# Optimization experiments

Hardware: AMD Instinct MI355X
Metric: run time of the kernel (lower is better)

## Reference

```python
import jax, jax.numpy as jnp
import numpy as np

B, T, C, H = 4, 2048, 768, 12
D = C // H  # head dim = 64
EPS = 1e-5


def setup_inputs() -> dict:
    key = jax.random.key(0)
    ks = jax.random.split(key, 12)
    s = lambda fan_in: 1.0 / np.sqrt(fan_in)
    return {
        "x": jax.random.normal(ks[0], (B, T, C), dtype=jnp.float32),
        "ln1_g": jnp.ones((C,), jnp.float32),
        "ln1_b": jnp.zeros((C,), jnp.float32),
        "w_attn": jax.random.normal(ks[1], (C, 3 * C), jnp.float32) * s(C),
        "b_attn": jnp.zeros((3 * C,), jnp.float32),
        "w_aproj": jax.random.normal(ks[2], (C, C), jnp.float32) * s(C),
        "b_aproj": jnp.zeros((C,), jnp.float32),
        "ln2_g": jnp.ones((C,), jnp.float32),
        "ln2_b": jnp.zeros((C,), jnp.float32),
        "w_fc": jax.random.normal(ks[3], (C, 4 * C), jnp.float32) * s(C),
        "b_fc": jnp.zeros((4 * C,), jnp.float32),
        "w_mproj": jax.random.normal(ks[4], (4 * C, C), jnp.float32) * s(4 * C),
        "b_mproj": jnp.zeros((C,), jnp.float32),
    }


def _layernorm(x, g, b):
    mu = jnp.mean(x, axis=-1, keepdims=True)
    var = jnp.mean(jnp.square(x - mu), axis=-1, keepdims=True)
    return (x - mu) * jax.lax.rsqrt(var + EPS) * g + b


def _attention(h, w_attn, b_attn, w_aproj, b_aproj):
    qkv = h @ w_attn + b_attn                          # [B,T,3C]
    q, k, v = jnp.split(qkv, 3, axis=-1)
    q = q.reshape(B, T, H, D)
    k = k.reshape(B, T, H, D)
    v = v.reshape(B, T, H, D)
    att = jnp.einsum("bqhd,bkhd->bhqk", q, k) * (1.0 / np.sqrt(D))
    causal = jnp.tril(jnp.ones((T, T), bool))
    att = jnp.where(causal, att, -jnp.inf)
    att = jax.nn.softmax(att, axis=-1)
    y = jnp.einsum("bhqk,bkhd->bqhd", att, v).reshape(B, T, C)
    return y @ w_aproj + b_aproj


def reference(x, ln1_g, ln1_b, w_attn, b_attn, w_aproj, b_aproj,
              ln2_g, ln2_b, w_fc, b_fc, w_mproj, b_mproj):
    x = x + _attention(_layernorm(x, ln1_g, ln1_b), w_attn, b_attn, w_aproj, b_aproj)
    h = _layernorm(x, ln2_g, ln2_b)
    h = jax.nn.gelu(h @ w_fc + b_fc, approximate=True)  # tanh approximation, matches F.gelu(approximate='tanh')
    x = x + (h @ w_mproj + b_mproj)
    return x
```

## Files before the change

kernel.cpp:

```cpp
#include <hip/hip_runtime.h>


typedef unsigned short ushortT;
typedef unsigned int uintT;
typedef __attribute__((ext_vector_type(8))) __bf16 bf16x8;
typedef __attribute__((ext_vector_type(4))) float f32x4;

#define MFMA16(a, b, c) __builtin_amdgcn_mfma_f32_16x16x32_bf16(a, b, c, 0, 0, 0)

__device__ inline float b2f(ushortT u) {
  return __uint_as_float(((uintT)u) << 16);
}
__device__ inline ushortT f2b(float f) {
  uintT x = __float_as_uint(f);
  uintT r = x + 0x7fffu + ((x >> 16) & 1u);
  return (ushortT)(r >> 16);
}
__device__ inline uintT pack_bf2(float a, float b) {
  return __builtin_amdgcn_perm(__float_as_uint(b), __float_as_uint(a),
                               0x07060302u);
}

__device__ inline float fast_exp2(float x) {
#if __has_builtin(__builtin_amdgcn_exp2f)
  return __builtin_amdgcn_exp2f(x);
#else
  return exp2f(x);
#endif
}

__device__ inline float gelu_tanh(float v) {
  float t = 0.7978845608028654f * (v + 0.044715f * v * v * v);
  return v / (1.0f + __expf(-2.0f * t));
}

__device__ __forceinline__ void glds16(const ushortT* g, ushortT* l) {
  __builtin_amdgcn_global_load_lds(
      (const __attribute__((address_space(1))) unsigned int*)(const void*)g,
      (__attribute__((address_space(3))) unsigned int*)(void*)l, 16, 0, 0);
}

__global__ __launch_bounds__(256) void detect_dtype(
    const ushortT* __restrict__ w, int* __restrict__ flag) {
  __shared__ int red;
  if (threadIdx.x == 0) red = 0;
  __syncthreads();
  int crazy = 0;
  for (int i = threadIdx.x; i < 4096; i += 256) {
    uintT e = (w[2 * i] >> 7) & 0xFF;
    if (e >= 150) crazy = 1;
  }
  if (crazy) atomicOr(&red, 1);
  __syncthreads();
  if (threadIdx.x == 0) *flag = red;
}

struct VecArgs {
  const void* src[8];
  int n[8];
  int dstoff[8];
};
__global__ __launch_bounds__(256) void convert_vecs(
    VecArgs a, ushortT* __restrict__ pv, const int* __restrict__ flag) {
  int fl = *flag;
  int t = blockIdx.y;
  int i = blockIdx.x * 256 + threadIdx.x;
  if (i >= a.n[t]) return;
  float v = fl ? ((const float*)a.src[t])[i] : b2f(((const ushortT*)a.src[t])[i]);
  pv[a.dstoff[t] + i] = f2b(v);
}

__global__ __launch_bounds__(256) void transpose_any(
    const void* __restrict__ in, ushortT* __restrict__ out, int K, int N,
    const int* __restrict__ flag) {
  __shared__ ushortT t[32][33];
  int fl = *flag;
  int n0 = blockIdx.x * 32, k0 = blockIdx.y * 32;
  int x = threadIdx.x, y0 = threadIdx.y;
#pragma unroll
  for (int i = y0; i < 32; i += 8) {
    size_t idx = (size_t)(k0 + i) * N + n0 + x;
    t[i][x] = fl ? f2b(((const float*)in)[idx]) : ((const ushortT*)in)[idx];
  }
  __syncthreads();
#pragma unroll
  for (int i = y0; i < 32; i += 8)
    out[(size_t)(n0 + i) * K + k0 + x] = t[x][i];
}

__global__ __launch_bounds__(256) void vtrans_kernel(
    const ushortT* __restrict__ qkv, ushortT* __restrict__ vt) {
  const int T = 2048, C3 = 2304;
  __shared__ ushortT tile[64][65];
  int bh = blockIdx.y;
  int b = bh / 12, h = bh % 12;
  int t0 = blockIdx.x * 64;
  int col = threadIdx.x & 63, rowi = threadIdx.x >> 6;
#pragma unroll
  for (int rr = rowi; rr < 64; rr += 4)
    tile[rr][col] =
        qkv[((size_t)(b * T + t0 + rr)) * C3 + 1536 + h * 64 + col];
  __syncthreads();
#pragma unroll
  for (int dd = rowi; dd < 64; dd += 4)
    vt[((size_t)bh * 64 + dd) * T + t0 + col] = tile[col][dd];
}

template <int MODE>
__global__ __launch_bounds__(256) void ln_kernel(
    const void* __restrict__ xin, const ushortT* __restrict__ g,
    const ushortT* __restrict__ bb, ushortT* __restrict__ out,
    const int* __restrict__ flag) {
  const int C = 768;
  bool f32;
  if constexpr (MODE == 1) f32 = true; else f32 = (*flag != 0);
  size_t base = (size_t)blockIdx.x * C;
  int tid = threadIdx.x;
  const float* xf = (const float*)xin;
  const ushortT* xb = (const ushortT*)xin;
  float v0 = f32 ? xf[base + tid]       : b2f(xb[base + tid]);
  float v1 = f32 ? xf[base + tid + 256] : b2f(xb[base + tid + 256]);
  float v2 = f32 ? xf[base + tid + 512] : b2f(xb[base + tid + 512]);
  float s = v0 + v1 + v2;
  float q = v0 * v0 + v1 * v1 + v2 * v2;
#pragma unroll
  for (int off = 32; off; off >>= 1) {
    s += __shfl_xor(s, off);
    q += __shfl_xor(q, off);
  }
  __shared__ float as_[4], aq_[4];
  if ((tid & 63) == 0) { as_[tid >> 6] = s; aq_[tid >> 6] = q; }
  __syncthreads();
  s = as_[0] + as_[1] + as_[2] + as_[3];
  q = aq_[0] + aq_[1] + aq_[2] + aq_[3];
  float mu = s * (1.0f / 768.0f);
  float var = q * (1.0f / 768.0f) - mu * mu;
  float rs = rsqrtf(var + 1e-5f);
  ushortT* orow = out + base;
  orow[tid]       = f2b((v0 - mu) * rs * b2f(g[tid])       + b2f(bb[tid]));
  orow[tid + 256] = f2b((v1 - mu) * rs * b2f(g[tid + 256]) + b2f(bb[tid + 256]));
  orow[tid + 512] = f2b((v2 - mu) * rs * b2f(g[tid + 512]) + b2f(bb[tid + 512]));
}

template <int EPI>
__global__ __launch_bounds__(256) void gemm_sb(
    const ushortT* __restrict__ A, const ushortT* __restrict__ Bt,
    const ushortT* __restrict__ bias, const void* __restrict__ res,
    void* __restrict__ out, int N, int K, int nbm, int nbn,
    const int* __restrict__ flag) {
  __shared__ ushortT As[128 * 64];
  __shared__ ushortT Bs[128 * 64];
  int fl = (EPI >= 2) ? *flag : 0;
  int tid = threadIdx.x;
  int lane = tid & 63, wave = tid >> 6;
  int quad = lane >> 4, n = lane & 15, n7 = n & 7;
  int wm = (wave >> 1) * 64, wn = (wave & 1) * 64;
  int l = blockIdx.x;
  int xcd = l & 7, j = l >> 3;
  int m0 = (xcd * (nbm >> 3) + j / nbn) * 128;
  int n0 = (j % nbn) * 128;

  int trow = tid >> 3;
  int tc = ((tid & 7) ^ (trow & 7)) << 3;
  const ushortT* ga = A + (size_t)(m0 + trow) * K + tc;
  const ushortT* gb = Bt + (size_t)(n0 + trow) * K + tc;
  const int ldst = wave * 512;

  const int c0 = (quad ^ n7) << 3;
  const int c1 = ((4 + quad) ^ n7) << 3;
  const int arow = (wm + n) * 64;
  const int brow = (wn + n) * 64;

  f32x4 acc[4][4] = {};

  for (int k0 = 0; k0 < K; k0 += 64) {
    __syncthreads();
#pragma unroll
    for (int i = 0; i < 4; ++i)
      glds16(ga + (size_t)(i * 32) * K + k0, As + ldst + i * 2048);
#pragma unroll
    for (int i = 0; i < 4; ++i)
      glds16(gb + (size_t)(i * 32) * K + k0, Bs + ldst + i * 2048);
    __syncthreads();

    bf16x8 af[4][2], bfr[4][2];
#pragma unroll
    for (int mi = 0; mi < 4; ++mi) {
      af[mi][0] = *(const bf16x8*)(As + arow + mi * 1024 + c0);
      af[mi][1] = *(const bf16x8*)(As + arow + mi * 1024 + c1);
    }
#pragma unroll
    for (int ni = 0; ni < 4; ++ni) {
      bfr[ni][0] = *(const bf16x8*)(Bs + brow + ni * 1024 + c0);
      bfr[ni][1] = *(const bf16x8*)(Bs + brow + ni * 1024 + c1);
    }
#pragma unroll
    for (int mi = 0; mi < 4; ++mi)
#pragma unroll
      for (int ni = 0; ni < 4; ++ni) {
        acc[mi][ni] = MFMA16(af[mi][0], bfr[ni][0], acc[mi][ni]);
        acc[mi][ni] = MFMA16(af[mi][1], bfr[ni][1], acc[mi][ni]);
      }
  }

#pragma unroll
  for (int mi = 0; mi < 4; ++mi) {
#pragma unroll
    for (int ni = 0; ni < 4; ++ni) {
      int gc = n0 + wn + ni * 16 + n;
      float bv = b2f(bias[gc]);
      int gr0 = m0 + wm + mi * 16 + quad * 4;
#pragma unroll
      for (int r = 0; r < 4; ++r) {
        size_t idx = (size_t)(gr0 + r) * N + gc;
        float v = acc[mi][ni][r] + bv;
        if constexpr (EPI == 1) v = gelu_tanh(v);
        if constexpr (EPI == 2) {
          v += fl ? ((const float*)res)[idx] : b2f(((const ushortT*)res)[idx]);
          ((float*)out)[idx] = v;
        } else if constexpr (EPI == 3) {
          v += ((const float*)res)[idx];
          if (fl) ((float*)out)[idx] = v;
          else    ((ushortT*)out)[idx] = f2b(v);
        } else {
          ((ushortT*)out)[idx] = f2b(v);
        }
      }
    }
  }
}

__global__ __launch_bounds__(256) void attn_kernel(
    const ushortT* __restrict__ qkv, const ushortT* __restrict__ vt,
    ushortT* __restrict__ y) {
  const int T = 2048, C3 = 2304;
  constexpr int LDP = 72;
  __shared__ ushortT Ks[2][64 * 64];
  __shared__ ushortT Vs[2][64 * 64];
  __shared__ ushortT Ps[4 * 16 * LDP];
  int bh = blockIdx.y;
  int b = bh / 12, h = bh % 12;
  int pj = blockIdx.x;
  int tid = threadIdx.x;
  int lane = tid & 63, wave = tid >> 6;
  int quad = lane >> 4, n = lane & 15, n7 = n & 7;

  const ushortT* base = qkv + (size_t)b * T * C3;
  const ushortT* kbase = base + 768 + h * 64;
  const ushortT* vbase = vt + (size_t)bh * 64 * T;
  ushortT* myP = Ps + wave * 16 * LDP;

  const float QS = 0.18033688011112042f;
  const float MB = 20.0f;

  int qtA = pj, qtB = 31 - pj;
  int nA = qtA + 1, ntot = 33;

  int srow = lane >> 3, scol = lane & 7;
  const ushortT* kg =
      kbase + (size_t)(wave * 16 + srow) * C3 + ((scol ^ srow) << 3);
  const ushortT* vg =
      vbase + (size_t)(wave * 16 + srow) * T + ((scol ^ srow) << 3);

  const int c0 = (quad ^ n7) << 3;
  const int c1 = ((4 + quad) ^ n7) << 3;

  int qt = qtA;
  int qw = qt * 64 + wave * 16;
  bf16x8 aq[2];
  {
    const ushortT* qrow = base + (size_t)(qw + n) * C3 + h * 64 + quad * 8;
#pragma unroll
    for (int dh = 0; dh < 2; ++dh) {
      union { ushortT u[8]; bf16x8 v; } tmp;
#pragma unroll
      for (int j = 0; j < 8; ++j) tmp.u[j] = f2b(b2f(qrow[dh * 32 + j]) * QS);
      aq[dh] = tmp.v;
    }
  }
  f32x4 Ot[4] = {};
  float l_ = 0.f;

  auto stage = [&](int kt_, int buf) {
    int kof = kt_ << 6;
    ushortT* lk = &Ks[buf][0] + wave * 1024;
    ushortT* lv = &Vs[buf][0] + wave * 1024;
    glds16(kg + (size_t)kof * C3, lk);
    glds16(kg + (size_t)(kof + 8) * C3, lk + 512);
    glds16(vg + kof, lv);
    glds16(vg + (size_t)8 * T + kof, lv + 512);
  };

  stage(0, 0);
  __syncthreads();

  int cur = 0;
  for (int t = 0; t < ntot; ++t) {
    int kt = (t < nA) ? t : t - nA;
    if (t + 1 < ntot) {
      int ktn = (t + 1 < nA) ? t + 1 : t + 1 - nA;
      stage(ktn, cur ^ 1);
    }
    const ushortT* ks = &Ks[cur][0];
    const ushortT* vs = &Vs[cur][0];

    f32x4 St[4];
#pragma unroll
    for (int g = 0; g < 4; ++g) {
      bf16x8 ka0 = *(const bf16x8*)(ks + (g * 16 + n) * 64 + c0);
      bf16x8 ka1 = *(const bf16x8*)(ks + (g * 16 + n) * 64 + c1);
      f32x4 z = {};
      z = MFMA16(ka0, aq[0], z);
      St[g] = MFMA16(ka1, aq[1], z);
    }
    if (kt == qt) {
      int lim = wave * 16 + n;
#pragma unroll
      for (int g = 0; g < 4; ++g)
#pragma unroll
        for (int r = 0; r < 4; ++r)
          if (g * 16 + quad * 4 + r > lim) St[g][r] = -1e30f;
    }
    float ls = 0.f;
#pragma unroll
    for (int g = 0; g < 4; ++g) {
      float p0 = fast_exp2(St[g][0] - MB);
      float p1 = fast_exp2(St[g][1] - MB);
      float p2 = fast_exp2(St[g][2] - MB);
      float p3 = fast_exp2(St[g][3] - MB);
      ls += (p0 + p1) + (p2 + p3);
      uint2 pk;
      pk.x = pack_bf2(p0, p1);
      pk.y = pack_bf2(p2, p3);
      *(uint2*)(myP + n * LDP + g * 16 + quad * 4) = pk;
    }
    ls += __shfl_xor(ls, 16);
    ls += __shfl_xor(ls, 32);
    l_ += ls;

    bf16x8 pb0 = *(const bf16x8*)(myP + n * LDP + quad * 8);
    bf16x8 pb1 = *(const bf16x8*)(myP + n * LDP + 32 + quad * 8);
#pragma unroll
    for (int dt = 0; dt < 4; ++dt) {
      bf16x8 va0 = *(const bf16x8*)(vs + (dt * 16 + n) * 64 + c0);
      bf16x8 va1 = *(const bf16x8*)(vs + (dt * 16 + n) * 64 + c1);
      Ot[dt] = MFMA16(va0, pb0, Ot[dt]);
      Ot[dt] = MFMA16(va1, pb1, Ot[dt]);
    }

    if (kt == qt) {
      float inv = 1.0f / l_;
      int qg = qw + n;
#pragma unroll
      for (int dt = 0; dt < 4; ++dt) {
        uint2 o;
        o.x = pack_bf2(Ot[dt][0] * inv, Ot[dt][1] * inv);
        o.y = pack_bf2(Ot[dt][2] * inv, Ot[dt][3] * inv);
        *(uint2*)(y + (size_t)(b * T + qg) * 768 + h * 64 + dt * 16 +
                  quad * 4) = o;
      }
      if (t + 1 < ntot) {
        qt = qtB;
        qw = qt * 64 + wave * 16;
        const ushortT* qrow =
            base + (size_t)(qw + n) * C3 + h * 64 + quad * 8;
#pragma unroll
        for (int dh = 0; dh < 2; ++dh) {
          union { ushortT u[8]; bf16x8 v; } tmp;
#pragma unroll
          for (int j = 0; j < 8; ++j)
            tmp.u[j] = f2b(b2f(qrow[dh * 32 + j]) * QS);
          aq[dh] = tmp.v;
        }
#pragma unroll
        for (int dt = 0; dt < 4; ++dt)
#pragma unroll
          for (int r = 0; r < 4; ++r) Ot[dt][r] = 0.f;
        l_ = 0.f;
      }
    }
    __syncthreads();
    cur ^= 1;
  }
}

extern "C" void kernel_launch(void* const* d_in, const int* in_sizes, int n_in,
                              void* d_out, int out_size, void* d_ws,
                              size_t ws_size, hipStream_t stream) {
  (void)in_sizes; (void)n_in; (void)out_size; (void)ws_size;
  const void* x       = d_in[0];
  const void* w_attn  = d_in[3];
  const void* w_aproj = d_in[5];
  const void* w_fc    = d_in[9];
  const void* w_mproj = d_in[11];

  char* ws = (char*)d_ws;
  ushortT* h1  = (ushortT*)(ws);
  ushortT* qkv = (ushortT*)(ws + 12582912);
  ushortT* yb  = (ushortT*)(ws + 50331648);
  float*   x1  = (float*)(ws + 62914560);
  ushortT* fcg = (ushortT*)(ws + 88080384);
  ushortT* wT0 = (ushortT*)(ws + 138412032);
  ushortT* wT1 = (ushortT*)(ws + 141950976);
  ushortT* wT2 = (ushortT*)(ws + 143130624);
  ushortT* wT3 = (ushortT*)(ws + 147849216);
  ushortT* pv  = (ushortT*)(ws + 152567808);
  int*     flag = (int*)(ws + 152600576);
  ushortT* vt  = h1;
  ushortT* h2  = yb;

  const int O_LN1G = 0, O_LN1B = 768, O_BATT = 1536, O_BAPR = 3840,
            O_LN2G = 4608, O_LN2B = 5376, O_BFC = 6144, O_BMPR = 9216;

  detect_dtype<<<1, 256, 0, stream>>>((const ushortT*)w_fc, flag);

  VecArgs va;
  va.src[0] = d_in[1];  va.n[0] = 768;  va.dstoff[0] = O_LN1G;
  va.src[1] = d_in[2];  va.n[1] = 768;  va.dstoff[1] = O_LN1B;
  va.src[2] = d_in[4];  va.n[2] = 2304; va.dstoff[2] = O_BATT;
  va.src[3] = d_in[6];  va.n[3] = 768;  va.dstoff[3] = O_BAPR;
  va.src[4] = d_in[7];  va.n[4] = 768;  va.dstoff[4] = O_LN2G;
  va.src[5] = d_in[8];  va.n[5] = 768;  va.dstoff[5] = O_LN2B;
  va.src[6] = d_in[10]; va.n[6] = 3072; va.dstoff[6] = O_BFC;
  va.src[7] = d_in[12]; va.n[7] = 768;  va.dstoff[7] = O_BMPR;
  convert_vecs<<<dim3(12, 8), 256, 0, stream>>>(va, pv, flag);

  dim3 tb(32, 8);
  transpose_any<<<dim3(72, 24), tb, 0, stream>>>(w_attn, wT0, 768, 2304, flag);
  transpose_any<<<dim3(24, 24), tb, 0, stream>>>(w_aproj, wT1, 768, 768, flag);
  transpose_any<<<dim3(96, 24), tb, 0, stream>>>(w_fc, wT2, 768, 3072, flag);
  transpose_any<<<dim3(24, 96), tb, 0, stream>>>(w_mproj, wT3, 3072, 768, flag);

  ln_kernel<0><<<8192, 256, 0, stream>>>(x, pv + O_LN1G, pv + O_LN1B, h1, flag);
  gemm_sb<0><<<1152, 256, 0, stream>>>(
      h1, wT0, pv + O_BATT, nullptr, qkv, 2304, 768, 64, 18, flag);
  vtrans_kernel<<<dim3(32, 48), 256, 0, stream>>>(qkv, vt);
  attn_kernel<<<dim3(16, 48), 256, 0, stream>>>(qkv, vt, yb);
  gemm_sb<2><<<384, 256, 0, stream>>>(
      yb, wT1, pv + O_BAPR, x, x1, 768, 768, 64, 6, flag);
  ln_kernel<1><<<8192, 256, 0, stream>>>(x1, pv + O_LN2G, pv + O_LN2B, h2, flag);
  gemm_sb<1><<<1536, 256, 0, stream>>>(
      h2, wT2, pv + O_BFC, nullptr, fcg, 3072, 768, 64, 24, flag);
  gemm_sb<3><<<384, 256, 0, stream>>>(
      fcg, wT3, pv + O_BMPR, x1, d_out, 768, 3072, 64, 6, flag);
}
```

Baseline: 438.0 us.

## Replace GEMM with triple-buffered pipelined kernel and wider 128x256 tiles

Replaces the single-buffered GEMM with one that cycles three LDS buffers over 32-wide K tiles. The next-but-one tile's global-to-LDS loads are issued while MFMAs run on the current tile, with explicit vmcnt waits and raised wave priority around the MFMAs. The QKV and FC GEMMs move to 128x256 block tiles with occupancy hinted at two blocks per CU. This aims to hide global load latency and improve operand reuse, at the cost of more LDS, more registers and more complex barrier and waitcnt logic.

```diff
diff --git a/kernel.cpp b/kernel.cpp
--- a/kernel.cpp
+++ b/kernel.cpp
@@ -142,71 +142,128 @@
   orow[tid + 512] = f2b((v2 - mu) * rs * b2f(g[tid + 512]) + b2f(bb[tid + 512]));
 }
 
-template <int EPI>
-__global__ __launch_bounds__(256) void gemm_sb(
+template <int EPI, int BN>
+__global__ __launch_bounds__(256, 2) void gemm_8p(
     const ushortT* __restrict__ A, const ushortT* __restrict__ Bt,
     const ushortT* __restrict__ bias, const void* __restrict__ res,
     void* __restrict__ out, int N, int K, int nbm, int nbn,
     const int* __restrict__ flag) {
-  __shared__ ushortT As[128 * 64];
-  __shared__ ushortT Bs[128 * 64];
+  constexpr int MI = (BN == 256) ? 8 : 4;
+  constexpr int NI = 4;
+  constexpr int LOADS = 2 + BN / 64;
+  __shared__ ushortT As3[3][128 * 32];
+  __shared__ ushortT Bs3[3][BN * 32];
   int fl = (EPI >= 2) ? *flag : 0;
   int tid = threadIdx.x;
   int lane = tid & 63, wave = tid >> 6;
-  int quad = lane >> 4, n = lane & 15, n7 = n & 7;
-  int wm = (wave >> 1) * 64, wn = (wave & 1) * 64;
+  int quad = lane >> 4, n = lane & 15;
+  int wm, wn;
+  if constexpr (BN == 256) { wm = 0; wn = wave * 64; }
+  else { wm = (wave >> 1) * 64; wn = (wave & 1) * 64; }
   int l = blockIdx.x;
   int xcd = l & 7, j = l >> 3;
   int m0 = (xcd * (nbm >> 3) + j / nbn) * 128;
-  int n0 = (j % nbn) * 128;
-
-  int trow = tid >> 3;
-  int tc = ((tid & 7) ^ (trow & 7)) << 3;
+  int n0 = (j % nbn) * BN;
+
+  int trow = tid >> 2;
+  int tc = (((tid & 3) ^ ((trow >> 1) & 3)) << 3);
   const ushortT* ga = A + (size_t)(m0 + trow) * K + tc;
   const ushortT* gb = Bt + (size_t)(n0 + trow) * K + tc;
-  const int ldst = wave * 512;
-
-  const int c0 = (quad ^ n7) << 3;
-  const int c1 = ((4 + quad) ^ n7) << 3;
-  const int arow = (wm + n) * 64;
-  const int brow = (wn + n) * 64;
-
-  f32x4 acc[4][4] = {};
-
-  for (int k0 = 0; k0 < K; k0 += 64) {
-    __syncthreads();
+
+  const int cs = (quad ^ ((n >> 1) & 3)) << 3;
+
+  int kt = K >> 5;
+  f32x4 acc[MI][NI] = {};
+
+  auto stage = [&](int tt, int slot) {
+    int k0 = tt << 5;
+    ushortT* la = &As3[slot][0] + wave * 512;
+    ushortT* lb = &Bs3[slot][0] + wave * 512;
+    glds16(ga + k0, la);
+    glds16(ga + (size_t)64 * K + k0, la + 2048);
+    glds16(gb + k0, lb);
+    glds16(gb + (size_t)64 * K + k0, lb + 2048);
+    if constexpr (BN == 256) {
+      glds16(gb + (size_t)128 * K + k0, lb + 4096);
+      glds16(gb + (size_t)192 * K + k0, lb + 6144);
+    }
+  };
+
+  stage(0, 0);
+  stage(1, 1);
+  if constexpr (BN == 256)
+    asm volatile("s_waitcnt vmcnt(6)" ::: "memory");
+  else
+    asm volatile("s_waitcnt vmcnt(4)" ::: "memory");
+  __builtin_amdgcn_s_barrier();
+
+  int cur = 0;
+  for (int t = 0; t < kt; ++t) {
+    const ushortT* ca = &As3[cur][0];
+    const ushortT* cb = &Bs3[cur][0];
+    int nxt = cur + 2; if (nxt >= 3) nxt -= 3;
+    bool pf = (t + 2) < kt;
+    int pk0 = (t + 2) << 5;
+    ushortT* la = &As3[nxt][0] + wave * 512;
+    ushortT* lb = &Bs3[nxt][0] + wave * 512;
+
+    bf16x8 af[4], bfr[NI];
 #pragma unroll
     for (int i = 0; i < 4; ++i)
-      glds16(ga + (size_t)(i * 32) * K + k0, As + ldst + i * 2048);
-#pragma unroll
-    for (int i = 0; i < 4; ++i)
-      glds16(gb + (size_t)(i * 32) * K + k0, Bs + ldst + i * 2048);
-    __syncthreads();
-
-    bf16x8 af[4][2], bfr[4][2];
-#pragma unroll
-    for (int mi = 0; mi < 4; ++mi) {
-      af[mi][0] = *(const bf16x8*)(As + arow + mi * 1024 + c0);
-      af[mi][1] = *(const bf16x8*)(As + arow + mi * 1024 + c1);
-    }
-#pragma unroll
-    for (int ni = 0; ni < 4; ++ni) {
-      bfr[ni][0] = *(const bf16x8*)(Bs + brow + ni * 1024 + c0);
-      bfr[ni][1] = *(const bf16x8*)(Bs + brow + ni * 1024 + c1);
-    }
+      af[i] = *(const bf16x8*)(ca + (wm + i * 16 + n) * 32 + cs);
+#pragma unroll
+    for (int i = 0; i < NI; ++i)
+      bfr[i] = *(const bf16x8*)(cb + (wn + i * 16 + n) * 32 + cs);
+    if (pf) {
+      glds16(ga + pk0, la);
+      glds16(ga + (size_t)64 * K + pk0, la + 2048);
+      glds16(gb + pk0, lb);
+      if constexpr (BN == 128) glds16(gb + (size_t)64 * K + pk0, lb + 2048);
+    }
+    __builtin_amdgcn_s_barrier();
+    __builtin_amdgcn_s_setprio(1);
 #pragma unroll
     for (int mi = 0; mi < 4; ++mi)
 #pragma unroll
-      for (int ni = 0; ni < 4; ++ni) {
-        acc[mi][ni] = MFMA16(af[mi][0], bfr[ni][0], acc[mi][ni]);
-        acc[mi][ni] = MFMA16(af[mi][1], bfr[ni][1], acc[mi][ni]);
+      for (int ni = 0; ni < NI; ++ni)
+        acc[mi][ni] = MFMA16(af[mi], bfr[ni], acc[mi][ni]);
+    __builtin_amdgcn_s_setprio(0);
+    if constexpr (BN == 256) {
+      __builtin_amdgcn_s_barrier();
+#pragma unroll
+      for (int i = 0; i < 4; ++i)
+        af[i] = *(const bf16x8*)(ca + (64 + i * 16 + n) * 32 + cs);
+      if (pf) {
+        glds16(gb + (size_t)64 * K + pk0, lb + 2048);
+        glds16(gb + (size_t)128 * K + pk0, lb + 4096);
+        glds16(gb + (size_t)192 * K + pk0, lb + 6144);
       }
-  }
-
-#pragma unroll
-  for (int mi = 0; mi < 4; ++mi) {
-#pragma unroll
-    for (int ni = 0; ni < 4; ++ni) {
+      __builtin_amdgcn_s_barrier();
+      __builtin_amdgcn_s_setprio(1);
+#pragma unroll
+      for (int mi = 0; mi < 4; ++mi)
+#pragma unroll
+        for (int ni = 0; ni < NI; ++ni)
+          acc[4 + mi][ni] = MFMA16(af[mi], bfr[ni], acc[4 + mi][ni]);
+      __builtin_amdgcn_s_setprio(0);
+    }
+    if (pf) {
+      if constexpr (BN == 256)
+        asm volatile("s_waitcnt vmcnt(6)" ::: "memory");
+      else
+        asm volatile("s_waitcnt vmcnt(4)" ::: "memory");
+    } else {
+      asm volatile("s_waitcnt vmcnt(0)" ::: "memory");
+    }
+    __builtin_amdgcn_s_barrier();
+
+    cur = cur + 1; if (cur == 3) cur = 0;
+  }
+
+#pragma unroll
+  for (int mi = 0; mi < MI; ++mi) {
+#pragma unroll
+    for (int ni = 0; ni < NI; ++ni) {
       int gc = n0 + wn + ni * 16 + n;
       float bv = b2f(bias[gc]);
       int gr0 = m0 + wm + mi * 16 + quad * 4;
@@ -432,15 +489,15 @@
   transpose_any<<<dim3(24, 96), tb, 0, stream>>>(w_mproj, wT3, 3072, 768, flag);
 
   ln_kernel<0><<<8192, 256, 0, stream>>>(x, pv + O_LN1G, pv + O_LN1B, h1, flag);
-  gemm_sb<0><<<1152, 256, 0, stream>>>(
-      h1, wT0, pv + O_BATT, nullptr, qkv, 2304, 768, 64, 18, flag);
+  gemm_8p<0, 256><<<576, 256, 0, stream>>>(
+      h1, wT0, pv + O_BATT, nullptr, qkv, 2304, 768, 64, 9, flag);
   vtrans_kernel<<<dim3(32, 48), 256, 0, stream>>>(qkv, vt);
   attn_kernel<<<dim3(16, 48), 256, 0, stream>>>(qkv, vt, yb);
-  gemm_sb<2><<<384, 256, 0, stream>>>(
+  gemm_8p<2, 128><<<384, 256, 0, stream>>>(
       yb, wT1, pv + O_BAPR, x, x1, 768, 768, 64, 6, flag);
   ln_kernel<1><<<8192, 256, 0, stream>>>(x1, pv + O_LN2G, pv + O_LN2B, h2, flag);
-  gemm_sb<1><<<1536, 256, 0, stream>>>(
-      h2, wT2, pv + O_BFC, nullptr, fcg, 3072, 768, 64, 24, flag);
-  gemm_sb<3><<<384, 256, 0, stream>>>(
+  gemm_8p<1, 256><<<768, 256, 0, stream>>>(
+      h2, wT2, pv + O_BFC, nullptr, fcg, 3072, 768, 64, 12, flag);
+  gemm_8p<3, 128><<<384, 256, 0, stream>>>(
       fcg, wT3, pv + O_BMPR, x1, d_out, 768, 3072, 64, 6, flag);
 }
```

Result: faster. 419.1 us (-4.3%).
